# Optimization experiments

Measured on AMD Instinct MI355X. Metric: run time of the kernel, lower is better.

The kernel has to match this reference:

```python
import jax, jax.numpy as jnp
import numpy as np

N_NODES = 100000
N_EDGES = 600000
HIDDEN = 128


def setup_inputs() -> dict:
    key = jax.random.key(0)
    ks = jax.random.split(key, 5)
    x = jax.random.normal(ks[0], (N_NODES, HIDDEN), dtype=jnp.float32)
    edge_index = jax.random.randint(ks[1], (2, N_EDGES), 0, N_NODES, dtype=jnp.int64)
    edge_weight = jax.random.uniform(ks[2], (N_EDGES,), dtype=jnp.float32)
    # MLP params: Linear(2*H+1 -> H), ReLU, Linear(H -> 1)
    W1 = jax.random.normal(ks[3], (2 * HIDDEN + 1, HIDDEN), dtype=jnp.float32) * (1.0 / np.sqrt(2 * HIDDEN + 1))
    b1 = jnp.zeros((HIDDEN,), dtype=jnp.float32)
    W2 = jax.random.normal(ks[4], (HIDDEN, 1), dtype=jnp.float32) * (1.0 / np.sqrt(HIDDEN))
    b2 = jnp.zeros((1,), dtype=jnp.float32)
    return {"x": x, "edge_index": edge_index, "edge_weight": edge_weight,
            "W1": W1, "b1": b1, "W2": W2, "b2": b2}


def reference(x, edge_index, edge_weight, W1, b1, W2, b2):
    num_nodes = x.shape[0]
    src = edge_index[0]
    tgt = edge_index[1]
    h_src = x[src]                      # [E, H] gather
    h_tgt = x[tgt]                      # [E, H] gather
    w = edge_weight[:, None]            # [E, 1]
    concat = jnp.concatenate([h_src, h_tgt, w], axis=-1)   # [E, 2H+1]
    hidden = jax.nn.relu(concat @ W1 + b1)                 # [E, H]
    scores = (hidden @ W2 + b2)[:, 0]                      # [E]
    # NOTE: the original _softmax_edge's max-pass uses index_put_(accumulate=True)
    # on a -inf buffer, so every touched entry stays -inf and is then replaced by 0;
    # the net effect is NO max subtraction. Faithful math: plain exp / segment_sum.
    exp_scores = jnp.exp(scores)
    sum_exp = jax.ops.segment_sum(exp_scores, tgt, num_segments=num_nodes)
    sum_exp = jnp.maximum(sum_exp, 1e-12)
    alpha = exp_scores / sum_exp[tgt]                      # [E]
    out = jax.ops.segment_sum(alpha[:, None] * h_src, tgt, num_segments=num_nodes)
    return x + out
```

## Files before the change

kernel.cpp:

```cpp
#include <hip/hip_runtime.h>
#include <hip/hip_bf16.h>

#define N_NODES 100000
#define N_EDGES 600000
#define HID 128
#define SCAN_NB 391
#define GEMM_BLOCKS 1563
#define FILL_BLOCKS 586


typedef short bf16x8 __attribute__((ext_vector_type(8)));
typedef float f32x4  __attribute__((ext_vector_type(4)));

__device__ inline unsigned short f2bf(float v) {
    __hip_bfloat16 h = __float2bfloat16(v);
    return *(unsigned short*)&h;
}
__device__ inline float2 bfpair(unsigned int u) {
    float lo = __uint_as_float(u << 16);
    float hi = __uint_as_float(u & 0xffff0000u);
    return make_float2(lo, hi);
}

__global__ __launch_bounds__(256) void k_prep(const float* __restrict__ W1,
                                              unsigned short* __restrict__ Bh,
                                              int* __restrict__ deg)
{
    int idx = blockIdx.x * 256 + threadIdx.x;
    if (idx < N_NODES) deg[idx] = 0;
    if (idx < 32768) {
        int n = idx & 255;
        int k = idx >> 8;
        float v = (n < HID) ? W1[k * HID + n] : W1[(HID + k) * HID + (n - HID)];
        Bh[(k >> 5) * 8192 + n * 32 + (k & 31)] = f2bf(v);
    }
}

__global__ __launch_bounds__(256) void k_count(const int* __restrict__ ei,
                                               int* __restrict__ deg)
{
    int e = blockIdx.x * blockDim.x + threadIdx.x;
    if (e < N_EDGES) atomicAdd(&deg[ei[N_EDGES + e]], 1);
}

__global__ __launch_bounds__(256) void k_partial(const int* __restrict__ deg,
                                                 int* __restrict__ partial)
{
    __shared__ int s[256];
    int t = threadIdx.x;
    int idx = blockIdx.x * 256 + t;
    s[t] = (idx < N_NODES) ? deg[idx] : 0;
    __syncthreads();
    #pragma unroll
    for (int off = 128; off > 0; off >>= 1) {
        if (t < off) s[t] += s[t + off];
        __syncthreads();
    }
    if (t == 0) partial[blockIdx.x] = s[0];
}

__global__ __launch_bounds__(256) void k_rowptr(const int* __restrict__ deg,
                                                const int* __restrict__ partial,
                                                int* __restrict__ rowptr,
                                                int* __restrict__ cursor)
{
    __shared__ int sp[256];
    __shared__ int s[256];
    int t = threadIdx.x;
    int b = blockIdx.x;

    int acc = 0;
    for (int i = t; i < b; i += 256) acc += partial[i];
    sp[t] = acc;
    __syncthreads();
    #pragma unroll
    for (int off = 128; off > 0; off >>= 1) {
        if (t < off) sp[t] += sp[t + off];
        __syncthreads();
    }
    int pb = sp[0];

    int idx = b * 256 + t;
    int v = (idx < N_NODES) ? deg[idx] : 0;
    s[t] = v;
    __syncthreads();
    #pragma unroll
    for (int off = 1; off < 256; off <<= 1) {
        int u = (t >= off) ? s[t - off] : 0;
        __syncthreads();
        s[t] += u;
        __syncthreads();
    }
    if (idx < N_NODES) {
        int r = pb + s[t] - v;
        rowptr[idx] = r;
        cursor[idx] = r;
    }
    if (idx == 0) rowptr[N_NODES] = N_EDGES;
}

__global__ __launch_bounds__(256) void k_gemm_fill(const float* __restrict__ x,
                                                   const unsigned short* __restrict__ BhG,
                                                   unsigned short* __restrict__ zbuf,
                                                   unsigned short* __restrict__ y2buf,
                                                   const int* __restrict__ ei,
                                                   const float* __restrict__ ew,
                                                   int* __restrict__ cursor,
                                                   uint2* __restrict__ eprs)
{
    __shared__ unsigned short Ah[64 * 32];

    if (blockIdx.x >= GEMM_BLOCKS) {
        int fb = blockIdx.x - GEMM_BLOCKS;
        for (int e = fb * 256 + threadIdx.x; e < N_EDGES; e += FILL_BLOCKS * 256) {
            int tgt = ei[N_EDGES + e];
            int pos = atomicAdd(&cursor[tgt], 1);
            eprs[pos] = make_uint2((unsigned int)ei[e], __float_as_uint(ew[e]));
        }
        return;
    }

    const int tid  = threadIdx.x;
    const int bm   = blockIdx.x * 64;
    const int wave = tid >> 6;
    const int lane = tid & 63;
    const int q    = lane >> 4;
    const int ln   = lane & 15;

    const int rowA = tid >> 3;
    const int rowB = rowA + 32;
    const int f4   = tid & 7;
    const int gmA  = bm + rowA;
    const int gmB  = bm + rowB;
    const bool okA = gmA < N_NODES;
    const bool okB = gmB < N_NODES;
    const float* pxA = &x[(size_t)gmA * HID + f4 * 4];
    const float* pxB = &x[(size_t)gmB * HID + f4 * 4];

    f32x4 acc[4][4] = {};

    float4 vA = make_float4(0.f,0.f,0.f,0.f), vB = vA;
    float4 vAn = vA, vBn = vA;
    if (okA) vA = *(const float4*)pxA;
    if (okB) vB = *(const float4*)pxB;

    for (int ks = 0; ks < 4; ++ks) {
        const int k0 = ks * 32;
        {
            float4 v = vA;
            unsigned int ph0 = (unsigned int)f2bf(v.x) | ((unsigned int)f2bf(v.y) << 16);
            unsigned int ph1 = (unsigned int)f2bf(v.z) | ((unsigned int)f2bf(v.w) << 16);
            *(uint2*)&Ah[rowA * 32 + f4 * 4] = make_uint2(ph0, ph1);
            if (okA) *(uint2*)&zbuf[(size_t)gmA * 256 + 128 + k0 + f4 * 4] = make_uint2(ph0, ph1);
        }
        {
            float4 v = vB;
            unsigned int ph0 = (unsigned int)f2bf(v.x) | ((unsigned int)f2bf(v.y) << 16);
            unsigned int ph1 = (unsigned int)f2bf(v.z) | ((unsigned int)f2bf(v.w) << 16);
            *(uint2*)&Ah[rowB * 32 + f4 * 4] = make_uint2(ph0, ph1);
            if (okB) *(uint2*)&zbuf[(size_t)gmB * 256 + 128 + k0 + f4 * 4] = make_uint2(ph0, ph1);
        }
        __syncthreads();

        if (ks < 3) {
            vAn = okA ? *(const float4*)(pxA + (ks + 1) * 32) : make_float4(0.f,0.f,0.f,0.f);
            vBn = okB ? *(const float4*)(pxB + (ks + 1) * 32) : make_float4(0.f,0.f,0.f,0.f);
        }

        bf16x8 ah[4], bh[4];
        #pragma unroll
        for (int mt = 0; mt < 4; ++mt) {
            ah[mt] = *(const bf16x8*)&Ah[(mt * 16 + ln) * 32 + q * 8];
        }
        #pragma unroll
        for (int nt = 0; nt < 4; ++nt) {
            bh[nt] = *(const bf16x8*)&BhG[ks * 8192 + (wave * 64 + nt * 16 + ln) * 32 + q * 8];
        }
        #pragma unroll
        for (int mt = 0; mt < 4; ++mt) {
            #pragma unroll
            for (int nt = 0; nt < 4; ++nt) {
                acc[mt][nt] = __builtin_amdgcn_mfma_f32_16x16x32_bf16(bh[nt], ah[mt], acc[mt][nt], 0, 0, 0);
            }
        }
        __syncthreads();
        vA = vAn; vB = vBn;
    }

    #pragma unroll
    for (int mt = 0; mt < 4; ++mt) {
        int node = bm + mt * 16 + ln;
        if (node < N_NODES) {
            #pragma unroll
            for (int nt = 0; nt < 4; ++nt) {
                int col0 = wave * 64 + nt * 16 + q * 4;
                unsigned int lo = (unsigned int)f2bf(acc[mt][nt][0]) | ((unsigned int)f2bf(acc[mt][nt][1]) << 16);
                unsigned int hi = (unsigned int)f2bf(acc[mt][nt][2]) | ((unsigned int)f2bf(acc[mt][nt][3]) << 16);
                if (col0 < 128) *(uint2*)&zbuf[(size_t)node * 256 + col0] = make_uint2(lo, hi);
                else            *(uint2*)&y2buf[(size_t)node * 128 + (col0 - 128)] = make_uint2(lo, hi);
            }
        }
    }
}

__global__ __launch_bounds__(256) void k_fused(const unsigned int* __restrict__ zu,
                                               const unsigned int* __restrict__ y2u,
                                               const int* __restrict__ rowptr,
                                               const uint2* __restrict__ eprs,
                                               const float* __restrict__ x,
                                               const float* __restrict__ W1,
                                               const float* __restrict__ b1,
                                               const float* __restrict__ W2,
                                               const float* __restrict__ b2,
                                               float* __restrict__ out)
{
    int n = (blockIdx.x * blockDim.x + threadIdx.x) >> 6;
    int lane = threadIdx.x & 63;
    if (n >= N_NODES) return;
    int ql = lane & 15;
    int qi = lane >> 4;
    int c0 = ql * 8;

    uint4 uy2 = *(const uint4*)&y2u[(size_t)n * 64 + ql * 4];
    float2 y2a = bfpair(uy2.x), y2b = bfpair(uy2.y), y2c = bfpair(uy2.z), y2d = bfpair(uy2.w);
    float4 bv0 = *(const float4*)&b1[c0];
    float4 bv1 = *(const float4*)&b1[c0 + 4];
    float4 wr0 = *(const float4*)&W1[256 * HID + c0];
    float4 wr1 = *(const float4*)&W1[256 * HID + c0 + 4];
    float4 w20 = *(const float4*)&W2[c0];
    float4 w21 = *(const float4*)&W2[c0 + 4];
    float p0 = y2a.x + bv0.x, p1 = y2a.y + bv0.y, p2 = y2b.x + bv0.z, p3 = y2b.y + bv0.w;
    float p4 = y2c.x + bv1.x, p5 = y2c.y + bv1.y, p6 = y2d.x + bv1.z, p7 = y2d.y + bv1.w;
    float b2v = b2[0];

    int beg = rowptr[n], end = rowptr[n + 1];
    float a0 = 0.f, a1 = 0.f, a2 = 0.f, a3 = 0.f;
    float a4 = 0.f, a5 = 0.f, a6 = 0.f, a7 = 0.f;
    float denom = 0.f;

    for (int i = beg; i < end; i += 4) {
        int idx = i + qi;
        bool valid = idx < end;
        int ie = valid ? idx : (end - 1);
        uint2 ep = eprs[ie];
        size_t base = (size_t)ep.x * 128;
        float w = __uint_as_float(ep.y);
        uint4 uy = *(const uint4*)&zu[base + ql * 4];
        uint4 ux = *(const uint4*)&zu[base + 64 + ql * 4];

        float2 ya = bfpair(uy.x), yb = bfpair(uy.y), yc = bfpair(uy.z), yd = bfpair(uy.w);
        float h0 = fmaxf(fmaf(w, wr0.x, ya.x + p0), 0.f);
        float h1 = fmaxf(fmaf(w, wr0.y, ya.y + p1), 0.f);
        float h2 = fmaxf(fmaf(w, wr0.z, yb.x + p2), 0.f);
        float h3 = fmaxf(fmaf(w, wr0.w, yb.y + p3), 0.f);
        float h4 = fmaxf(fmaf(w, wr1.x, yc.x + p4), 0.f);
        float h5 = fmaxf(fmaf(w, wr1.y, yc.y + p5), 0.f);
        float h6 = fmaxf(fmaf(w, wr1.z, yd.x + p6), 0.f);
        float h7 = fmaxf(fmaf(w, wr1.w, yd.y + p7), 0.f);
        float s = ((h0 * w20.x + h1 * w20.y) + (h2 * w20.z + h3 * w20.w))
                + ((h4 * w21.x + h5 * w21.y) + (h6 * w21.z + h7 * w21.w));
        #pragma unroll
        for (int m = 1; m <= 8; m <<= 1) s += __shfl_xor(s, m, 64);
        float es = valid ? __expf(s + b2v) : 0.f;

        float2 xa = bfpair(ux.x), xb = bfpair(ux.y), xc = bfpair(ux.z), xd = bfpair(ux.w);
        a0 = fmaf(es, xa.x, a0); a1 = fmaf(es, xa.y, a1);
        a2 = fmaf(es, xb.x, a2); a3 = fmaf(es, xb.y, a3);
        a4 = fmaf(es, xc.x, a4); a5 = fmaf(es, xc.y, a5);
        a6 = fmaf(es, xd.x, a6); a7 = fmaf(es, xd.y, a7);
        denom += es;
    }

    #pragma unroll
    for (int m = 16; m <= 32; m <<= 1) {
        a0 += __shfl_xor(a0, m, 64); a1 += __shfl_xor(a1, m, 64);
        a2 += __shfl_xor(a2, m, 64); a3 += __shfl_xor(a3, m, 64);
        a4 += __shfl_xor(a4, m, 64); a5 += __shfl_xor(a5, m, 64);
        a6 += __shfl_xor(a6, m, 64); a7 += __shfl_xor(a7, m, 64);
        denom += __shfl_xor(denom, m, 64);
    }

    if (qi == 0) {
        float4 xt0 = *(const float4*)&x[(size_t)n * HID + c0];
        float4 xt1 = *(const float4*)&x[(size_t)n * HID + c0 + 4];
        float inv = 1.0f / fmaxf(denom, 1e-12f);
        float4 o0, o1;
        o0.x = xt0.x + a0 * inv; o0.y = xt0.y + a1 * inv;
        o0.z = xt0.z + a2 * inv; o0.w = xt0.w + a3 * inv;
        o1.x = xt1.x + a4 * inv; o1.y = xt1.y + a5 * inv;
        o1.z = xt1.z + a6 * inv; o1.w = xt1.w + a7 * inv;
        *(float4*)&out[(size_t)n * HID + c0]     = o0;
        *(float4*)&out[(size_t)n * HID + c0 + 4] = o1;
    }
}

extern "C" void kernel_launch(void* const* d_in, const int* in_sizes, int n_in,
                              void* d_out, int out_size, void* d_ws, size_t ws_size,
                              hipStream_t stream) {
    const float* x  = (const float*)d_in[0];
    const int*   ei = (const int*)d_in[1];
    const float* ew = (const float*)d_in[2];
    const float* W1 = (const float*)d_in[3];
    const float* b1 = (const float*)d_in[4];
    const float* W2 = (const float*)d_in[5];
    const float* b2 = (const float*)d_in[6];
    float* out = (float*)d_out;
    char* ws = (char*)d_ws;

    const size_t deg_b    = 400000;
    const size_t rowptr_b = 400016;
    const size_t cursor_b = 400000;
    const size_t eprs_b   = 4800000;
    const size_t part_b   = 1568;
    const size_t pb_b     = 1568;
    const size_t Bh_b     = 65536;

    char* p = ws;
    int* deg      = (int*)p;             p += deg_b;
    int* rowptr   = (int*)p;             p += rowptr_b;
    int* cursor   = (int*)p;             p += cursor_b;
    uint2* eprs   = (uint2*)p;           p += eprs_b;
    int* partial  = (int*)p;             p += part_b;
    p += pb_b;
    unsigned short* BhG = (unsigned short*)p;  p += Bh_b;
    unsigned short* zbuf  = (unsigned short*)p;  p += (size_t)N_NODES * 256 * 2;
    unsigned short* y2buf = (unsigned short*)p;

    const int edge_blocks = (N_EDGES + 255) / 256;
    const int node_wave_blocks = (N_NODES * 64 + 255) / 256;

    hipLaunchKernelGGL(k_prep,   dim3(SCAN_NB), dim3(256), 0, stream, W1, BhG, deg);
    hipLaunchKernelGGL(k_count,  dim3(edge_blocks), dim3(256), 0, stream, ei, deg);
    hipLaunchKernelGGL(k_partial,dim3(SCAN_NB), dim3(256), 0, stream, deg, partial);
    hipLaunchKernelGGL(k_rowptr, dim3(SCAN_NB), dim3(256), 0, stream, deg, partial, rowptr, cursor);
    hipLaunchKernelGGL(k_gemm_fill, dim3(GEMM_BLOCKS + FILL_BLOCKS), dim3(256), 0, stream,
                       x, BhG, zbuf, y2buf, ei, ew, cursor, eprs);
    hipLaunchKernelGGL(k_fused, dim3(node_wave_blocks), dim3(256), 0, stream,
                       (const unsigned int*)zbuf, (const unsigned int*)y2buf,
                       rowptr, eprs, x, W1, b1, W2, b2, out);
}
```

Measured before the change: 270.0 us.

## Merge scan kernels, schedule fill blocks first, use lighter LDS barriers

Drops the separate partial-sum kernel: each rowptr block now sums all preceding degrees directly, saving one launch but adding redundant reads that grow with block index. The CSR fill blocks are moved to the front of the combined GEMM/fill grid so the atomic-heavy scatter starts early. __syncthreads in the GEMM loop is replaced by an LDS-only waitcnt plus s_barrier, so the barrier does not wait on outstanding global loads and prefetches.

```diff
diff --git a/kernel.cpp b/kernel.cpp
--- a/kernel.cpp
+++ b/kernel.cpp
@@ -20,6 +20,10 @@
     float lo = __uint_as_float(u << 16);
     float hi = __uint_as_float(u & 0xffff0000u);
     return make_float2(lo, hi);
+}
+__device__ inline void lds_barrier() {
+    asm volatile("s_waitcnt lgkmcnt(0)" ::: "memory");
+    __builtin_amdgcn_s_barrier();
 }
 
 __global__ __launch_bounds__(256) void k_prep(const float* __restrict__ W1,
@@ -43,44 +47,28 @@
     if (e < N_EDGES) atomicAdd(&deg[ei[N_EDGES + e]], 1);
 }
 
-__global__ __launch_bounds__(256) void k_partial(const int* __restrict__ deg,
-                                                 int* __restrict__ partial)
+__global__ __launch_bounds__(256) void k_rowptr(const int* __restrict__ deg,
+                                                int* __restrict__ rowptr,
+                                                int* __restrict__ cursor)
 {
     __shared__ int s[256];
     int t = threadIdx.x;
-    int idx = blockIdx.x * 256 + t;
-    s[t] = (idx < N_NODES) ? deg[idx] : 0;
+    int b = blockIdx.x;
+    int lim = b * 256;
+
+    int acc = 0;
+    for (int i = t; i < lim; i += 256) acc += deg[i];
+    s[t] = acc;
     __syncthreads();
     #pragma unroll
     for (int off = 128; off > 0; off >>= 1) {
         if (t < off) s[t] += s[t + off];
         __syncthreads();
     }
-    if (t == 0) partial[blockIdx.x] = s[0];
-}
-
-__global__ __launch_bounds__(256) void k_rowptr(const int* __restrict__ deg,
-                                                const int* __restrict__ partial,
-                                                int* __restrict__ rowptr,
-                                                int* __restrict__ cursor)
-{
-    __shared__ int sp[256];
-    __shared__ int s[256];
-    int t = threadIdx.x;
-    int b = blockIdx.x;
-
-    int acc = 0;
-    for (int i = t; i < b; i += 256) acc += partial[i];
-    sp[t] = acc;
+    int pb = s[0];
     __syncthreads();
-    #pragma unroll
-    for (int off = 128; off > 0; off >>= 1) {
-        if (t < off) sp[t] += sp[t + off];
-        __syncthreads();
-    }
-    int pb = sp[0];
-
-    int idx = b * 256 + t;
+
+    int idx = lim + t;
     int v = (idx < N_NODES) ? deg[idx] : 0;
     s[t] = v;
     __syncthreads();
@@ -110,8 +98,8 @@
 {
     __shared__ unsigned short Ah[64 * 32];
 
-    if (blockIdx.x >= GEMM_BLOCKS) {
-        int fb = blockIdx.x - GEMM_BLOCKS;
+    if (blockIdx.x < FILL_BLOCKS) {
+        int fb = blockIdx.x;
         for (int e = fb * 256 + threadIdx.x; e < N_EDGES; e += FILL_BLOCKS * 256) {
             int tgt = ei[N_EDGES + e];
             int pos = atomicAdd(&cursor[tgt], 1);
@@ -121,7 +109,7 @@
     }
 
     const int tid  = threadIdx.x;
-    const int bm   = blockIdx.x * 64;
+    const int bm   = (blockIdx.x - FILL_BLOCKS) * 64;
     const int wave = tid >> 6;
     const int lane = tid & 63;
     const int q    = lane >> 4;
@@ -160,7 +148,7 @@
             *(uint2*)&Ah[rowB * 32 + f4 * 4] = make_uint2(ph0, ph1);
             if (okB) *(uint2*)&zbuf[(size_t)gmB * 256 + 128 + k0 + f4 * 4] = make_uint2(ph0, ph1);
         }
-        __syncthreads();
+        lds_barrier();
 
         if (ks < 3) {
             vAn = okA ? *(const float4*)(pxA + (ks + 1) * 32) : make_float4(0.f,0.f,0.f,0.f);
@@ -183,7 +171,7 @@
                 acc[mt][nt] = __builtin_amdgcn_mfma_f32_16x16x32_bf16(bh[nt], ah[mt], acc[mt][nt], 0, 0, 0);
             }
         }
-        __syncthreads();
+        lds_barrier();
         vA = vAn; vB = vBn;
     }
 
@@ -320,7 +308,7 @@
     int* rowptr   = (int*)p;             p += rowptr_b;
     int* cursor   = (int*)p;             p += cursor_b;
     uint2* eprs   = (uint2*)p;           p += eprs_b;
-    int* partial  = (int*)p;             p += part_b;
+    p += part_b;
     p += pb_b;
     unsigned short* BhG = (unsigned short*)p;  p += Bh_b;
     unsigned short* zbuf  = (unsigned short*)p;  p += (size_t)N_NODES * 256 * 2;
@@ -331,8 +319,7 @@
 
     hipLaunchKernelGGL(k_prep,   dim3(SCAN_NB), dim3(256), 0, stream, W1, BhG, deg);
     hipLaunchKernelGGL(k_count,  dim3(edge_blocks), dim3(256), 0, stream, ei, deg);
-    hipLaunchKernelGGL(k_partial,dim3(SCAN_NB), dim3(256), 0, stream, deg, partial);
-    hipLaunchKernelGGL(k_rowptr, dim3(SCAN_NB), dim3(256), 0, stream, deg, partial, rowptr, cursor);
+    hipLaunchKernelGGL(k_rowptr, dim3(SCAN_NB), dim3(256), 0, stream, deg, rowptr, cursor);
     hipLaunchKernelGGL(k_gemm_fill, dim3(GEMM_BLOCKS + FILL_BLOCKS), dim3(256), 0, stream,
                        x, BhG, zbuf, y2buf, ei, ew, cursor, eprs);
     hipLaunchKernelGGL(k_fused, dim3(node_wave_blocks), dim3(256), 0, stream,
```

New measurement: 323.8 us. 19.9% more time.
